# Optimization experiments

Hardware: AMD Instinct MI355X
Metric: run time of the kernel (lower is better)

## Reference

```python
import jax, jax.numpy as jnp
import numpy as np


def fps(xyz, npoint):
    # xyz: [B, N, 3] -> idx [B, npoint]; iterative farthest point sampling (start at index 0)
    B, N, _ = xyz.shape
    dist0 = jnp.full((B, N), 1e10, xyz.dtype)
    far0 = jnp.zeros((B,), jnp.int32)
    def body(carry, _):
        dist, far = carry
        centroid = jnp.take_along_axis(xyz, far[:, None, None], axis=1)  # [B,1,3]
        d = jnp.sum((xyz - centroid) ** 2, axis=-1)                      # [B,N]
        dist = jnp.minimum(dist, d)
        return (dist, jnp.argmax(dist, axis=-1).astype(jnp.int32)), far
    _, idx = jax.lax.scan(body, (dist0, far0), None, length=npoint)
    return idx.T  # [B, npoint]


def ball_query(radius, nsample, xyz, new_xyz):
    # xyz [B,N,3], new_xyz [B,S,3] -> idx [B,S,nsample]
    B, S, _ = new_xyz.shape
    N = xyz.shape[1]
    sqr = jnp.sum((new_xyz[:, :, None, :] - xyz[:, None, :, :]) ** 2, axis=-1)  # [B,S,N]
    idx = jnp.broadcast_to(jnp.arange(N, dtype=jnp.int32), (B, S, N))
    idx = jnp.where(sqr > radius * radius, N, idx)
    idx = jnp.sort(idx, axis=-1)[:, :, :nsample]
    first = idx[:, :, :1]
    return jnp.where(idx == N, first, idx)


def index_points(points, idx):
    # points [B,N,C], idx [B,...] int -> [B,...,C]
    B = points.shape[0]
    out = jnp.take_along_axis(points, idx.reshape(B, -1, 1), axis=1)
    return out.reshape(idx.shape + (points.shape[-1],))


def set_abstraction(xyz, points, npoint, radius, nsample, ws, bs):
    fidx = fps(xyz, npoint)
    new_xyz = index_points(xyz, fidx)                       # [B,S,3]
    gidx = ball_query(radius, nsample, xyz, new_xyz)        # [B,S,ns]
    grouped = index_points(xyz, gidx) - new_xyz[:, :, None, :]  # centered neighbors
    if points is not None:
        grouped = jnp.concatenate([grouped, index_points(points, gidx)], axis=-1)
    x = grouped                                             # [B,S,ns,Cin]
    for w, b in zip(ws, bs):  # shared 1x1-conv MLP (eval-mode BN folded into w,b) + ReLU
        x = jax.nn.relu(jnp.einsum('bsnc,oc->bsno', x, w) + b)
    return new_xyz, jnp.max(x, axis=2)                      # max-pool over neighbors


def sa_group_all(xyz, points, ws, bs):
    x = jnp.concatenate([xyz, points], axis=-1)             # [B,N,3+C]
    for w, b in zip(ws, bs):
        x = jax.nn.relu(jnp.einsum('bnc,oc->bno', x, w) + b)
    return jnp.max(x, axis=1)                               # [B,1024]


def setup_inputs() -> dict:
    key = jax.random.key(0)
    ks = iter(jax.random.split(key, 64))
    def w(shape):
        return jax.random.normal(next(ks), shape, jnp.float32) * 0.02
    d = {"xyz": jax.random.normal(next(ks), (32, 3, 4096), jnp.float32)}
    mlps = {"s1": [(64, 3), (64, 64), (128, 64)],
            "s2": [(128, 131), (128, 128), (256, 128)],
            "s3": [(256, 259), (512, 256), (1024, 512)]}
    for name, layers in mlps.items():
        for i, (o, c) in enumerate(layers):
            d[name + "w" + str(i)] = w((o, c))
            d[name + "b" + str(i)] = jnp.zeros((o,), jnp.float32)
    for name, (o, c) in {"f1": (512, 1024), "f2": (256, 512), "f3": (6, 256)}.items():
        d[name + "w"] = w((o, c))
        d[name + "b"] = jnp.zeros((o,), jnp.float32)
    return d


def reference(xyz, s1w0, s1b0, s1w1, s1b1, s1w2, s1b2,
              s2w0, s2b0, s2w1, s2b1, s2w2, s2b2,
              s3w0, s3b0, s3w1, s3b1, s3w2, s3b2,
              f1w, f1b, f2w, f2b, f3w, f3b):
    pts = jnp.transpose(xyz, (0, 2, 1))  # [B,N,3]
    l1x, l1p = set_abstraction(pts, None, 512, 0.2, 32, [s1w0, s1w1, s1w2], [s1b0, s1b1, s1b2])
    l2x, l2p = set_abstraction(l1x, l1p, 128, 0.4, 64, [s2w0, s2w1, s2w2], [s2b0, s2b1, s2b2])
    feat = sa_group_all(l2x, l2p, [s3w0, s3w1, s3w2], [s3b0, s3b1, s3b2])  # [B,1024]
    x = jax.nn.relu(feat @ f1w.T + f1b)   # fc1 + (folded BN) + ReLU; dropout=identity (eval)
    x = jax.nn.relu(x @ f2w.T + f2b)
    return x @ f3w.T + f3b                # [B,6] value head (softmax=False)
```

## Files before the change

kernel.cpp:

```cpp
#include <hip/hip_runtime.h>
#include <hip/hip_bf16.h>


typedef __attribute__((ext_vector_type(8))) short short8;
typedef __attribute__((ext_vector_type(4))) float f32x4;
union SV8 { short8 v; ushort u[8]; };

__device__ __forceinline__ ushort f2bf(float x) {
    unsigned u = __float_as_uint(x);
    unsigned r = (u + 0x7fffu + ((u >> 16) & 1u)) >> 16;
    return (ushort)r;
}

template<int CTRL>
__device__ __forceinline__ unsigned long long dpp_mov_u64(unsigned long long x) {
    const int lo = (int)(unsigned)(x & 0xffffffffull);
    const int hi = (int)(unsigned)(x >> 32);
    const int nlo = __builtin_amdgcn_update_dpp(lo, lo, CTRL, 0xf, 0xf, false);
    const int nhi = __builtin_amdgcn_update_dpp(hi, hi, CTRL, 0xf, 0xf, false);
    return ((unsigned long long)(unsigned)nhi << 32) | (unsigned)nlo;
}

__device__ __forceinline__ unsigned long long wave_max_u64(unsigned long long x) {
    unsigned long long y;
    y = dpp_mov_u64<0x111>(x); if (y > x) x = y;
    y = dpp_mov_u64<0x112>(x); if (y > x) x = y;
    y = dpp_mov_u64<0x114>(x); if (y > x) x = y;
    y = dpp_mov_u64<0x118>(x); if (y > x) x = y;
    y = dpp_mov_u64<0x142>(x); if (y > x) x = y;
    y = dpp_mov_u64<0x143>(x); if (y > x) x = y;
    return x;
}

template<int N, int S, int NT, bool CHW>
__device__ __forceinline__ void fps_body(const float* __restrict__ xyz,
                                         float* __restrict__ new_xyz,
                                         int b, int t, char* smem) {
    constexpr int P  = N / NT;
    constexpr int NW = NT / 64;
    float4* sxyz = (float4*)smem;
    unsigned long long* rv = (unsigned long long*)(smem + (size_t)N * 16);
    int* sfar = (int*)(smem + (size_t)N * 16 + 2 * NW * 8);
    float px[P], py[P], pz[P], dist[P];
    unsigned idc[P];
    if (CHW) {
        const float* base = xyz + (size_t)b * 3 * N;
        #pragma unroll
        for (int p = 0; p < P; ++p) {
            const int i = p * NT + t;
            px[p] = base[i]; py[p] = base[N + i]; pz[p] = base[2 * N + i];
            sxyz[i] = make_float4(px[p], py[p], pz[p], 0.0f);
        }
    } else {
        const float* base = xyz + (size_t)b * N * 3;
        #pragma unroll
        for (int p = 0; p < P; ++p) {
            const int i = p * NT + t;
            px[p] = base[i*3]; py[p] = base[i*3+1]; pz[p] = base[i*3+2];
            sxyz[i] = make_float4(px[p], py[p], pz[p], 0.0f);
        }
    }
    #pragma unroll
    for (int p = 0; p < P; ++p) { dist[p] = 1e10f; idc[p] = (unsigned)(N - 1 - (p * NT + t)); }
    __syncthreads();
    int far = 0;
    for (int j = 0; j < S; ++j) {
        if (t == 0) sfar[j] = far;
        const float4 cen = sxyz[far];
        unsigned long long pk[P];
        #pragma unroll
        for (int p = 0; p < P; ++p) {
            const float dx = px[p] - cen.x, dy = py[p] - cen.y, dz = pz[p] - cen.z;
            const float d = __fadd_rn(__fadd_rn(__fmul_rn(dx, dx), __fmul_rn(dy, dy)), __fmul_rn(dz, dz));
            const float nd = fminf(dist[p], d);
            dist[p] = nd;
            pk[p] = ((unsigned long long)__float_as_uint(nd) << 32) | idc[p];
        }
        #pragma unroll
        for (int s = P / 2; s > 0; s >>= 1)
            #pragma unroll
            for (int k = 0; k < s; ++k)
                if (pk[k + s] > pk[k]) pk[k] = pk[k + s];
        unsigned long long best = wave_max_u64(pk[0]);
        if constexpr (NW > 1) {
            const int sl = (j & 1) * NW;
            if ((t & 63) == 63) rv[sl + (t >> 6)] = best;
            __syncthreads();
            unsigned long long bb = rv[sl];
            #pragma unroll
            for (int w = 1; w < NW; ++w) { const unsigned long long v = rv[sl + w]; if (v > bb) bb = v; }
            far = N - 1 - (int)(bb & 0xffffffffull);
        } else {
            far = N - 1 - __builtin_amdgcn_readlane((int)(best & 0xffffffffull), 63);
        }
    }
    __syncthreads();
    float* out = new_xyz + (size_t)b * S * 3;
    for (int i = t; i < S; i += NT) {
        const float4 c = sxyz[sfar[i]];
        out[i*3+0] = c.x; out[i*3+1] = c.y; out[i*3+2] = c.z;
    }
}

__device__ __forceinline__ void packg(const float* __restrict__ src,
                                      ushort* __restrict__ dh,
                                      int Ktot, int otiles, int cofs, int idx) {
    const int j = idx & 7, lane = (idx >> 3) & 63;
    const int ot = (idx >> 9) % otiles;
    const int ks = idx / (512 * otiles);
    const int m = lane & 15, q = lane >> 4;
    const int o = ot * 16 + m, c = cofs + ks * 32 + q * 8 + j;
    const float v = (c < Ktot) ? src[(size_t)o * Ktot + c] : 0.0f;
    dh[idx] = f2bf(v);
}

__global__ __launch_bounds__(256)
void fps1_prep_kernel(const float* __restrict__ xyz, float* __restrict__ l1xyz,
                 const float* s1w0, const float* s1b0, float4* Wc1,
                 const float* s1w1, ushort* M1W1h,
                 const float* s1w2, ushort* M1W2h,
                 const float* s3w0, ushort* S3W0h,
                 const float* s3w1, ushort* S3W1h,
                 const float* s3w2, ushort* S3W2h,
                 const float* s2w0, const float* s2b0, float4* Wc0,
                 ushort* W0h,
                 const float* s2w1, ushort* W1h,
                 const float* s2w2, ushort* W2h) {
    __shared__ __align__(16) char smem[4096 * 16 + 64 + 512 * 4];
    if (blockIdx.x < 32) {
        fps_body<4096, 512, 256, true>(xyz, l1xyz, blockIdx.x, threadIdx.x, smem);
        return;
    }
    int i = (blockIdx.x - 32) * 256 + threadIdx.x;
    if (i < 64)     { Wc1[i] = make_float4(s1w0[i*3], s1w0[i*3+1], s1w0[i*3+2], s1b0[i]); return; }  i -= 64;
    if (i < 4096)   { packg(s1w1, M1W1h,  64,  4, 0, i); return; }   i -= 4096;
    if (i < 8192)   { packg(s1w2, M1W2h,  64,  8, 0, i); return; }   i -= 8192;
    if (i < 73728)  { packg(s3w0, S3W0h, 259, 16, 0, i); return; }   i -= 73728;
    if (i < 131072) { packg(s3w1, S3W1h, 256, 32, 0, i); return; }   i -= 131072;
    if (i < 524288) { packg(s3w2, S3W2h, 512, 64, 0, i); return; }   i -= 524288;
    if (i < 16384)  { packg(s2w0, W0h, 131,  8, 3, i); return; }     i -= 16384;
    if (i < 16384)  { packg(s2w1, W1h, 128,  8, 0, i); return; }     i -= 16384;
    if (i < 32768)  { packg(s2w2, W2h, 128, 16, 0, i); return; }     i -= 32768;
    if (i < 128) {
        Wc0[i] = make_float4(s2w0[(size_t)i*131+0], s2w0[(size_t)i*131+1],
                             s2w0[(size_t)i*131+2], s2b0[i]);
    }
}

template<int N, int NS, bool CHW, int NT>
__global__ __launch_bounds__(NT)
void bq_kernel(float r2, const float* __restrict__ xyz, const float* __restrict__ cen,
               int* __restrict__ gidx, int S) {
    constexpr int WPB = NT / 64;
    __shared__ __align__(16) float4 sp[N];
    const int t = threadIdx.x, lane = t & 63, w = t >> 6;
    const int cen0 = blockIdx.x * WPB;
    const int b = cen0 / S;
    if (CHW) {
        const float* base = xyz + (size_t)b * 3 * N;
        for (int i = t; i < N; i += NT)
            sp[i] = make_float4(base[i], base[N + i], base[2 * N + i], 0.0f);
    } else {
        const float* base = xyz + (size_t)b * N * 3;
        for (int i = t; i < N; i += NT)
            sp[i] = make_float4(base[i*3], base[i*3+1], base[i*3+2], 0.0f);
    }
    __syncthreads();
    const int wid = cen0 + w;
    const float cx = cen[(size_t)wid*3+0], cy = cen[(size_t)wid*3+1], cz = cen[(size_t)wid*3+2];
    int* out = gidx + (size_t)wid * NS;
    int cnt = 0, first = -1;
    for (int b0 = 0; b0 < N; b0 += 64) {
        const float4 p = sp[b0 + lane];
        const float dx = p.x - cx, dy = p.y - cy, dz = p.z - cz;
        const float d = __fadd_rn(__fadd_rn(__fmul_rn(dx, dx), __fmul_rn(dy, dy)), __fmul_rn(dz, dz));
        const bool in = (d <= r2);
        const unsigned long long m = __ballot(in);
        if (first < 0 && m != 0ull) first = b0 + __ffsll((unsigned long long)m) - 1;
        const int pos = cnt + (int)__popcll(m & ((1ull << lane) - 1ull));
        if (in && pos < NS) out[pos] = b0 + lane;
        cnt += (int)__popcll(m);
        if (cnt >= NS) break;
    }
    if (cnt < NS)
        for (int k = cnt + lane; k < NS; k += 64) out[k] = first;
}

__global__ __launch_bounds__(256)
void mlp1_kernel(const float* __restrict__ xyz, const float* __restrict__ l1xyz,
                 float* __restrict__ l2xyz,
                 const int* __restrict__ gidx, const float4* __restrict__ Wc1,
                 const ushort* __restrict__ W1h, const float* __restrict__ b1,
                 const ushort* __restrict__ W2h, const float* __restrict__ b2,
                 float* __restrict__ l1p) {
    __shared__ __align__(16) char smem[64 * 68 * 4 * 2];
    float* bufA = (float*)smem;
    float* bufB = (float*)(smem + 64 * 68 * 4);
    const int t = threadIdx.x, b = blockIdx.y;
    if (blockIdx.x == 256) {
        fps_body<512, 128, 256, false>(l1xyz, l2xyz, b, t, smem);
        return;
    }
    const int s0 = blockIdx.x * 2;
    {
        const int n = t >> 2, c = t & 3;
        const int s = s0 + (n >> 5);
        const int gi = gidx[((size_t)b * 512 + s) * 32 + (n & 31)];
        float v = 0.0f;
        if (c < 3) v = xyz[(size_t)b * 3 * 4096 + c * 4096 + gi] - l1xyz[((size_t)b * 512 + s) * 3 + c];
        bufB[n * 4 + c] = v;
    }
    __syncthreads();
    {
        const int o = t & 63, ng = t >> 6;
        const float4 wc = Wc1[o];
        #pragma unroll
        for (int r = 0; r < 16; ++r) {
            const int n = ng * 16 + r;
            const float z = wc.w + wc.x * bufB[n*4] + wc.y * bufB[n*4+1] + wc.z * bufB[n*4+2];
            bufA[n * 68 + o] = fmaxf(z, 0.0f);
        }
    }
    const int lane = t & 63, wv = t >> 6;
    const int m = lane & 15, q = lane >> 4;
    const int rowA = wv * 16 + m;
    f32x4 acc1[4];
    #pragma unroll
    for (int ot = 0; ot < 4; ++ot)
        #pragma unroll
        for (int r = 0; r < 4; ++r) acc1[ot][r] = 0.0f;
    #pragma unroll
    for (int ks = 0; ks < 2; ++ks) {
        float xv[8];
        *(float4*)&xv[0] = *(const float4*)&bufA[rowA * 68 + ks * 32 + q * 8];
        *(float4*)&xv[4] = *(const float4*)&bufA[rowA * 68 + ks * 32 + q * 8 + 4];
        SV8 ah;
        #pragma unroll
        for (int j = 0; j < 8; ++j) ah.u[j] = f2bf(xv[j]);
        #pragma unroll
        for (int ot = 0; ot < 4; ++ot) {
            SV8 bh;
            bh.v = *(const short8*)(W1h + (size_t)((ks * 4 + ot) * 64 + lane) * 8);
            acc1[ot] = __builtin_amdgcn_mfma_f32_16x16x32_bf16(ah.v, bh.v, acc1[ot], 0, 0, 0);
        }
    }
    #pragma unroll
    for (int ot = 0; ot < 4; ++ot) {
        const float bb = b1[ot * 16 + m];
        #pragma unroll
        for (int r = 0; r < 4; ++r)
            bufB[(wv * 16 + q * 4 + r) * 68 + ot * 16 + m] = fmaxf(acc1[ot][r] + bb, 0.0f);
    }
    f32x4 acc2[8];
    #pragma unroll
    for (int ot = 0; ot < 8; ++ot)
        #pragma unroll
        for (int r = 0; r < 4; ++r) acc2[ot][r] = 0.0f;
    #pragma unroll
    for (int ks = 0; ks < 2; ++ks) {
        float xv[8];
        *(float4*)&xv[0] = *(const float4*)&bufB[rowA * 68 + ks * 32 + q * 8];
        *(float4*)&xv[4] = *(const float4*)&bufB[rowA * 68 + ks * 32 + q * 8 + 4];
        SV8 ah;
        #pragma unroll
        for (int j = 0; j < 8; ++j) ah.u[j] = f2bf(xv[j]);
        #pragma unroll
        for (int ot = 0; ot < 8; ++ot) {
            SV8 bh;
            bh.v = *(const short8*)(W2h + (size_t)((ks * 8 + ot) * 64 + lane) * 8);
            acc2[ot] = __builtin_amdgcn_mfma_f32_16x16x32_bf16(ah.v, bh.v, acc2[ot], 0, 0, 0);
        }
    }
    __syncthreads();
    #pragma unroll
    for (int ot = 0; ot < 8; ++ot) {
        const float bb = b2[ot * 16 + m];
        float mx = 0.0f;
        #pragma unroll
        for (int r = 0; r < 4; ++r) mx = fmaxf(mx, acc2[ot][r] + bb);
        bufA[(wv * 4 + q) * 128 + ot * 16 + m] = mx;
    }
    __syncthreads();
    {
        const int half = t >> 7, o = t & 127;
        float v = bufA[(half * 8) * 128 + o];
        #pragma unroll
        for (int rr = 1; rr < 8; ++rr) v = fmaxf(v, bufA[(half * 8 + rr) * 128 + o]);
        l1p[((size_t)b * 512 + s0 + half) * 128 + o] = v;
    }
}

__global__ __launch_bounds__(256)
void mlp2_kernel(const float* __restrict__ l1xyz, const float* __restrict__ l1p,
                 const float* __restrict__ l2xyz, const int* __restrict__ gidx,
                 const ushort* __restrict__ W0h, const float4* __restrict__ Wc0,
                 const ushort* __restrict__ W1h, const float* __restrict__ b1,
                 const ushort* __restrict__ W2h, const float* __restrict__ b2,
                 float* __restrict__ X3) {
    __shared__ __align__(16) float Abuf[64 * 132];
    __shared__ __align__(16) float Bbuf[64 * 132];
    __shared__ int sg[64];
    const int t = threadIdx.x, bs = blockIdx.x, b = bs >> 7;
    if (t < 64) sg[t] = gidx[(size_t)bs * 64 + t];
    if (t < 3)  X3[(size_t)bs * 288 + t] = l2xyz[(size_t)bs * 3 + t];
    if (t >= 64 && t < 93) X3[(size_t)bs * 288 + 259 + (t - 64)] = 0.0f;
    __syncthreads();
    for (int i = t; i < 64 * 32; i += 256) {
        const int n = i >> 5, cc = i & 31;
        *(float4*)&Abuf[n * 132 + cc * 4] =
            *(const float4*)&l1p[((size_t)b * 512 + sg[n]) * 128 + cc * 4];
    }
    if (t < 192) {
        const int n = t / 3, c = t % 3;
        Abuf[n * 132 + 128 + c] =
            l1xyz[((size_t)b * 512 + sg[n]) * 3 + c] - l2xyz[(size_t)bs * 3 + c];
    }
    __syncthreads();
    const int lane = t & 63, wv = t >> 6;
    const int m = lane & 15, q = lane >> 4;
    const int rowA = wv * 16 + m;

    f32x4 acc0[8];
    #pragma unroll
    for (int ot = 0; ot < 8; ++ot)
        #pragma unroll
        for (int r = 0; r < 4; ++r) acc0[ot][r] = 0.0f;
    #pragma unroll
    for (int ks = 0; ks < 4; ++ks) {
        float xv[8];
        *(float4*)&xv[0] = *(const float4*)&Abuf[rowA * 132 + ks * 32 + q * 8];
        *(float4*)&xv[4] = *(const float4*)&Abuf[rowA * 132 + ks * 32 + q * 8 + 4];
        SV8 ah;
        #pragma unroll
        for (int j = 0; j < 8; ++j) ah.u[j] = f2bf(xv[j]);
        #pragma unroll
        for (int ot = 0; ot < 8; ++ot) {
            SV8 bh;
            bh.v = *(const short8*)(W0h + (size_t)((ks * 8 + ot) * 64 + lane) * 8);
            acc0[ot] = __builtin_amdgcn_mfma_f32_16x16x32_bf16(ah.v, bh.v, acc0[ot], 0, 0, 0);
        }
    }
    float crd[4][3];
    #pragma unroll
    for (int r = 0; r < 4; ++r) {
        const int n = wv * 16 + q * 4 + r;
        crd[r][0] = Abuf[n * 132 + 128];
        crd[r][1] = Abuf[n * 132 + 129];
        crd[r][2] = Abuf[n * 132 + 130];
    }
    #pragma unroll
    for (int ot = 0; ot < 8; ++ot) {
        const float4 wc = Wc0[ot * 16 + m];
        #pragma unroll
        for (int r = 0; r < 4; ++r) {
            const float v = acc0[ot][r] + wc.w + wc.x * crd[r][0] + wc.y * crd[r][1] + wc.z * crd[r][2];
            Bbuf[(wv * 16 + q * 4 + r) * 132 + ot * 16 + m] = fmaxf(v, 0.0f);
        }
    }
    __syncthreads();

    f32x4 acc1[8];
    #pragma unroll
    for (int ot = 0; ot < 8; ++ot)
        #pragma unroll
        for (int r = 0; r < 4; ++r) acc1[ot][r] = 0.0f;
    #pragma unroll
    for (int ks = 0; ks < 4; ++ks) {
        float xv[8];
        *(float4*)&xv[0] = *(const float4*)&Bbuf[rowA * 132 + ks * 32 + q * 8];
        *(float4*)&xv[4] = *(const float4*)&Bbuf[rowA * 132 + ks * 32 + q * 8 + 4];
        SV8 ah;
        #pragma unroll
        for (int j = 0; j < 8; ++j) ah.u[j] = f2bf(xv[j]);
        #pragma unroll
        for (int ot = 0; ot < 8; ++ot) {
            SV8 bh;
            bh.v = *(const short8*)(W1h + (size_t)((ks * 8 + ot) * 64 + lane) * 8);
            acc1[ot] = __builtin_amdgcn_mfma_f32_16x16x32_bf16(ah.v, bh.v, acc1[ot], 0, 0, 0);
        }
    }
    __syncthreads();
    #pragma unroll
    for (int ot = 0; ot < 8; ++ot) {
        const float bb = b1[ot * 16 + m];
        #pragma unroll
        for (int r = 0; r < 4; ++r)
            Abuf[(wv * 16 + q * 4 + r) * 132 + ot * 16 + m] = fmaxf(acc1[ot][r] + bb, 0.0f);
    }
    __syncthreads();

    f32x4 acc2[16];
    #pragma unroll
    for (int ot = 0; ot < 16; ++ot)
        #pragma unroll
        for (int r = 0; r < 4; ++r) acc2[ot][r] = 0.0f;
    #pragma unroll
    for (int ks = 0; ks < 4; ++ks) {
        float xv[8];
        *(float4*)&xv[0] = *(const float4*)&Abuf[rowA * 132 + ks * 32 + q * 8];
        *(float4*)&xv[4] = *(const float4*)&Abuf[rowA * 132 + ks * 32 + q * 8 + 4];
        SV8 ah;
        #pragma unroll
        for (int j = 0; j < 8; ++j) ah.u[j] = f2bf(xv[j]);
        #pragma unroll
        for (int ot = 0; ot < 16; ++ot) {
            SV8 bh;
            bh.v = *(const short8*)(W2h + (size_t)((ks * 16 + ot) * 64 + lane) * 8);
            acc2[ot] = __builtin_amdgcn_mfma_f32_16x16x32_bf16(ah.v, bh.v, acc2[ot], 0, 0, 0);
        }
    }
    __syncthreads();
    #pragma unroll
    for (int ot = 0; ot < 16; ++ot) {
        const float bb = b2[ot * 16 + m];
        float mx = 0.0f;
        #pragma unroll
        for (int r = 0; r < 4; ++r) mx = fmaxf(mx, acc2[ot][r] + bb);
        Bbuf[(wv * 4 + q) * 256 + ot * 16 + m] = mx;
    }
    __syncthreads();
    {
        float v = Bbuf[t];
        #pragma unroll
        for (int rr = 1; rr < 16; ++rr) v = fmaxf(v, Bbuf[rr * 256 + t]);
        X3[(size_t)bs * 288 + 3 + t] = v;
    }
}

template<int KSTEPS, int OTILES, bool MAXOUT>
__global__ __launch_bounds__(256)
void gemm_mfma_kernel(const float* __restrict__ A, int AS,
                      const ushort* __restrict__ Wh,
                      const float* __restrict__ bias, float* __restrict__ C, int O) {
    __shared__ float part[16][OTILES * 16];
    const int t = threadIdx.x, lane = t & 63, wv = t >> 6;
    const int m = lane & 15, q = lane >> 4;
    const int rowA = blockIdx.x * 64 + wv * 16 + m;
    const int bo = blockIdx.y, OT = O >> 4;
    f32x4 acc[OTILES];
    #pragma unroll
    for (int ot = 0; ot < OTILES; ++ot)
        #pragma unroll
        for (int r = 0; r < 4; ++r) acc[ot][r] = 0.0f;
    for (int ks = 0; ks < KSTEPS; ++ks) {
        float xv[8];
        *(float4*)&xv[0] = *(const float4*)&A[(size_t)rowA * AS + ks * 32 + q * 8];
        *(float4*)&xv[4] = *(const float4*)&A[(size_t)rowA * AS + ks * 32 + q * 8 + 4];
        SV8 ah;
        #pragma unroll
        for (int j = 0; j < 8; ++j) ah.u[j] = f2bf(xv[j]);
        #pragma unroll
        for (int ot = 0; ot < OTILES; ++ot) {
            const size_t wb = (size_t)((ks * OT + bo * OTILES + ot) * 64 + lane) * 8;
            SV8 bh;
            bh.v = *(const short8*)(Wh + wb);
            acc[ot] = __builtin_amdgcn_mfma_f32_16x16x32_bf16(ah.v, bh.v, acc[ot], 0, 0, 0);
        }
    }
    if (!MAXOUT) {
        #pragma unroll
        for (int ot = 0; ot < OTILES; ++ot) {
            const int col = (bo * OTILES + ot) * 16 + m;
            const float bb = bias[col];
            #pragma unroll
            for (int r = 0; r < 4; ++r) {
                const int row = blockIdx.x * 64 + wv * 16 + q * 4 + r;
                C[(size_t)row * O + col] = fmaxf(acc[ot][r] + bb, 0.0f);
            }
        }
    } else {
        #pragma unroll
        for (int ot = 0; ot < OTILES; ++ot) {
            const int col = (bo * OTILES + ot) * 16 + m;
            const float bb = bias[col];
            float mx = 0.0f;
            #pragma unroll
            for (int r = 0; r < 4; ++r) mx = fmaxf(mx, acc[ot][r] + bb);
            part[wv * 4 + q][ot * 16 + m] = mx;
        }
        __syncthreads();
        for (int o = t; o < OTILES * 16; o += 256) {
            float v = part[0][o];
            #pragma unroll
            for (int rr = 1; rr < 16; ++rr) v = fmaxf(v, part[rr][o]);
            C[(size_t)blockIdx.x * O + bo * OTILES * 16 + o] = v;
        }
    }
}

__global__ __launch_bounds__(256)
void fchead_kernel(const float* __restrict__ P3,
                   const float* __restrict__ f1w, const float* __restrict__ f1b,
                   const float* __restrict__ f2w, const float* __restrict__ f2b,
                   const float* __restrict__ f3w, const float* __restrict__ f3b,
                   float* __restrict__ out) {
    __shared__ __align__(16) float x[1024];
    __shared__ __align__(16) float h1[512];
    __shared__ __align__(16) float h2[256];
    const int t = threadIdx.x, b = blockIdx.x;
    for (int i = t; i < 1024; i += 256)
        x[i] = fmaxf(P3[(size_t)(2*b)*1024 + i], P3[(size_t)(2*b+1)*1024 + i]);
    __syncthreads();
    #pragma unroll
    for (int oo = 0; oo < 2; ++oo) {
        const int o = t + oo * 256;
        const float4* wr = (const float4*)(f1w + (size_t)o * 1024);
        float s0 = 0, s1 = 0, s2 = 0, s3 = 0;
        for (int c = 0; c < 256; ++c) {
            const float4 w4 = wr[c];
            const float4 xv = *(const float4*)&x[c * 4];
            s0 += w4.x * xv.x; s1 += w4.y * xv.y; s2 += w4.z * xv.z; s3 += w4.w * xv.w;
        }
        h1[o] = fmaxf(f1b[o] + ((s0 + s1) + (s2 + s3)), 0.0f);
    }
    __syncthreads();
    {
        const float4* wr = (const float4*)(f2w + (size_t)t * 512);
        float s0 = 0, s1 = 0, s2 = 0, s3 = 0;
        for (int c = 0; c < 128; ++c) {
            const float4 w4 = wr[c];
            const float4 xv = *(const float4*)&h1[c * 4];
            s0 += w4.x * xv.x; s1 += w4.y * xv.y; s2 += w4.z * xv.z; s3 += w4.w * xv.w;
        }
        h2[t] = fmaxf(f2b[t] + ((s0 + s1) + (s2 + s3)), 0.0f);
    }
    __syncthreads();
    if (t < 6) {
        const float4* wr = (const float4*)(f3w + (size_t)t * 256);
        float s0 = 0, s1 = 0, s2 = 0, s3 = 0;
        for (int c = 0; c < 64; ++c) {
            const float4 w4 = wr[c];
            const float4 xv = *(const float4*)&h2[c * 4];
            s0 += w4.x * xv.x; s1 += w4.y * xv.y; s2 += w4.z * xv.z; s3 += w4.w * xv.w;
        }
        out[b * 6 + t] = f3b[t] + ((s0 + s1) + (s2 + s3));
    }
}

extern "C" void kernel_launch(void* const* d_in, const int* in_sizes, int n_in,
                              void* d_out, int out_size, void* d_ws, size_t ws_size,
                              hipStream_t stream) {
    const float* xyz  = (const float*)d_in[0];
    const float* s1w0 = (const float*)d_in[1];  const float* s1b0 = (const float*)d_in[2];
    const float* s1w1 = (const float*)d_in[3];  const float* s1b1 = (const float*)d_in[4];
    const float* s1w2 = (const float*)d_in[5];  const float* s1b2 = (const float*)d_in[6];
    const float* s2w0 = (const float*)d_in[7];  const float* s2b0 = (const float*)d_in[8];
    const float* s2w1 = (const float*)d_in[9];  const float* s2b1 = (const float*)d_in[10];
    const float* s2w2 = (const float*)d_in[11]; const float* s2b2 = (const float*)d_in[12];
    const float* s3w0 = (const float*)d_in[13]; const float* s3b0 = (const float*)d_in[14];
    const float* s3w1 = (const float*)d_in[15]; const float* s3b1 = (const float*)d_in[16];
    const float* s3w2 = (const float*)d_in[17]; const float* s3b2 = (const float*)d_in[18];
    const float* f1w  = (const float*)d_in[19]; const float* f1b  = (const float*)d_in[20];
    const float* f2w  = (const float*)d_in[21]; const float* f2b  = (const float*)d_in[22];
    const float* f3w  = (const float*)d_in[23]; const float* f3b  = (const float*)d_in[24];

    char* ws = (char*)d_ws;
    float* l1_xyz = (float*)(ws + 0);
    int*   gidx1  = (int*)  (ws + 196608);
    float* l1p    = (float*)(ws + 2293760);
    float* l2_xyz = (float*)(ws + 10682368);
    int*   gidx2  = (int*)  (ws + 10731520);
    float* X3p    = (float*)(ws + 11780096);
    const size_t PK = 16498688;
    float4* Wc1   = (float4*)(ws + PK + 0);
    ushort* M1W1h = (ushort*)(ws + PK + 1024);
    ushort* M1W2h = (ushort*)(ws + PK + 17408);
    ushort* W0h   = (ushort*)(ws + PK + 50176);
    ushort* W1h   = (ushort*)(ws + PK + 115712);
    ushort* W2h   = (ushort*)(ws + PK + 181248);
    float4* Wc0   = (float4*)(ws + PK + 312320);
    ushort* S3W0h = (ushort*)(ws + PK + 314368);
    ushort* S3W1h = (ushort*)(ws + PK + 609280);
    ushort* S3W2h = (ushort*)(ws + PK + 1133568);
    float* Y1   = (float*)(ws + 19729408);
    float* Y2   = (float*)(ws + 23923712);
    float* P3   = (float*)(ws + 32312320);

    fps1_prep_kernel<<<3186, 256, 0, stream>>>(xyz, l1_xyz,
        s1w0, s1b0, Wc1, s1w1, M1W1h, s1w2, M1W2h,
        s3w0, S3W0h, s3w1, S3W1h, s3w2, S3W2h,
        s2w0, s2b0, Wc0, W0h, s2w1, W1h, s2w2, W2h);
    bq_kernel<4096, 32, true, 1024><<<1024, 1024, 0, stream>>>(
        (float)(0.2 * 0.2), xyz, l1_xyz, gidx1, 512);
    {
        dim3 g(257, 32);
        mlp1_kernel<<<g, 256, 0, stream>>>(xyz, l1_xyz, l2_xyz, gidx1,
            Wc1, M1W1h, s1b1, M1W2h, s1b2, l1p);
    }

    bq_kernel<512, 64, false, 1024><<<256, 1024, 0, stream>>>(
        (float)(0.4 * 0.4), l1_xyz, l2_xyz, gidx2, 128);
    mlp2_kernel<<<4096, 256, 0, stream>>>(l1_xyz, l1p, l2_xyz, gidx2,
        W0h, Wc0, W1h, s2b1, W2h, s2b2, X3p);

    {
        dim3 g1(64, 4);
        gemm_mfma_kernel<9,  4, false><<<g1, 256, 0, stream>>>(X3p, 288, S3W0h, s3b0, Y1, 256);
        dim3 g2(64, 8);
        gemm_mfma_kernel<8,  4, false><<<g2, 256, 0, stream>>>(Y1, 256, S3W1h, s3b1, Y2, 512);
        dim3 g3(64, 16);
        gemm_mfma_kernel<16, 4, true ><<<g3, 256, 0, stream>>>(Y2, 512, S3W2h, s3b2, P3, 1024);
    }

    fchead_kernel<<<32, 256, 0, stream>>>(P3, f1w, f1b, f2w, f2b, f3w, f3b, (float*)d_out);
    (void)in_sizes; (void)n_in; (void)out_size; (void)ws_size;
}
```

Baseline: 783.0 us.

## Fuse three group-all MLP GEMMs into one kernel with LDS-resident bf16 intermediates

Replaces three separate MFMA GEMM launches for the global set-abstraction MLP with a single kernel. Each block processes 64 rows through all three layers and keeps the hidden activations in shared memory as bf16. The final max-pool is written directly. This removes the global round trips for the Y1/Y2 intermediates and two launches, but shrinks the grid to 64 blocks so each block does all output channels serially with lower parallelism.

```diff
diff --git a/kernel.cpp b/kernel.cpp
--- a/kernel.cpp
+++ b/kernel.cpp
@@ -427,64 +427,116 @@
     }
 }
 
-template<int KSTEPS, int OTILES, bool MAXOUT>
 __global__ __launch_bounds__(256)
-void gemm_mfma_kernel(const float* __restrict__ A, int AS,
-                      const ushort* __restrict__ Wh,
-                      const float* __restrict__ bias, float* __restrict__ C, int O) {
-    __shared__ float part[16][OTILES * 16];
+void fused3_kernel(const float* __restrict__ A,
+                   const ushort* __restrict__ W0h, const float* __restrict__ b0,
+                   const ushort* __restrict__ W1h, const float* __restrict__ b1,
+                   const ushort* __restrict__ W2h, const float* __restrict__ b2,
+                   float* __restrict__ P3) {
+    __shared__ __align__(16) char arena[64*264*2 + 64*520*2 + 16*256*4];
+    ushort* h1 = (ushort*)arena;
+    ushort* h2 = (ushort*)(arena + 64*264*2);
+    float* part = (float*)(arena + 64*264*2 + 64*520*2);
     const int t = threadIdx.x, lane = t & 63, wv = t >> 6;
     const int m = lane & 15, q = lane >> 4;
-    const int rowA = blockIdx.x * 64 + wv * 16 + m;
-    const int bo = blockIdx.y, OT = O >> 4;
-    f32x4 acc[OTILES];
-    #pragma unroll
-    for (int ot = 0; ot < OTILES; ++ot)
-        #pragma unroll
-        for (int r = 0; r < 4; ++r) acc[ot][r] = 0.0f;
-    for (int ks = 0; ks < KSTEPS; ++ks) {
-        float xv[8];
-        *(float4*)&xv[0] = *(const float4*)&A[(size_t)rowA * AS + ks * 32 + q * 8];
-        *(float4*)&xv[4] = *(const float4*)&A[(size_t)rowA * AS + ks * 32 + q * 8 + 4];
-        SV8 ah;
-        #pragma unroll
-        for (int j = 0; j < 8; ++j) ah.u[j] = f2bf(xv[j]);
-        #pragma unroll
-        for (int ot = 0; ot < OTILES; ++ot) {
-            const size_t wb = (size_t)((ks * OT + bo * OTILES + ot) * 64 + lane) * 8;
-            SV8 bh;
-            bh.v = *(const short8*)(Wh + wb);
-            acc[ot] = __builtin_amdgcn_mfma_f32_16x16x32_bf16(ah.v, bh.v, acc[ot], 0, 0, 0);
-        }
-    }
-    if (!MAXOUT) {
-        #pragma unroll
-        for (int ot = 0; ot < OTILES; ++ot) {
-            const int col = (bo * OTILES + ot) * 16 + m;
-            const float bb = bias[col];
-            #pragma unroll
-            for (int r = 0; r < 4; ++r) {
-                const int row = blockIdx.x * 64 + wv * 16 + q * 4 + r;
-                C[(size_t)row * O + col] = fmaxf(acc[ot][r] + bb, 0.0f);
+    const int rloc = wv * 16;
+    const size_t rowA = (size_t)blockIdx.x * 64 + rloc + m;
+
+    {
+        f32x4 acc[16];
+        #pragma unroll
+        for (int ot = 0; ot < 16; ++ot)
+            #pragma unroll
+            for (int r = 0; r < 4; ++r) acc[ot][r] = 0.0f;
+        #pragma unroll
+        for (int ks = 0; ks < 9; ++ks) {
+            float xv[8];
+            *(float4*)&xv[0] = *(const float4*)&A[rowA * 288 + ks * 32 + q * 8];
+            *(float4*)&xv[4] = *(const float4*)&A[rowA * 288 + ks * 32 + q * 8 + 4];
+            SV8 ah;
+            #pragma unroll
+            for (int j = 0; j < 8; ++j) ah.u[j] = f2bf(xv[j]);
+            #pragma unroll
+            for (int ot = 0; ot < 16; ++ot) {
+                SV8 bh;
+                bh.v = *(const short8*)(W0h + (size_t)((ks * 16 + ot) * 64 + lane) * 8);
+                acc[ot] = __builtin_amdgcn_mfma_f32_16x16x32_bf16(ah.v, bh.v, acc[ot], 0, 0, 0);
             }
         }
-    } else {
-        #pragma unroll
-        for (int ot = 0; ot < OTILES; ++ot) {
-            const int col = (bo * OTILES + ot) * 16 + m;
-            const float bb = bias[col];
+        #pragma unroll
+        for (int ot = 0; ot < 16; ++ot) {
+            const float bb = b0[ot * 16 + m];
+            #pragma unroll
+            for (int r = 0; r < 4; ++r)
+                h1[(rloc + q * 4 + r) * 264 + ot * 16 + m] = f2bf(fmaxf(acc[ot][r] + bb, 0.0f));
+        }
+    }
+    __syncthreads();
+
+    #pragma unroll
+    for (int og = 0; og < 2; ++og) {
+        f32x4 acc[16];
+        #pragma unroll
+        for (int ot = 0; ot < 16; ++ot)
+            #pragma unroll
+            for (int r = 0; r < 4; ++r) acc[ot][r] = 0.0f;
+        #pragma unroll
+        for (int ks = 0; ks < 8; ++ks) {
+            SV8 ah;
+            ah.v = *(const short8*)(h1 + (rloc + m) * 264 + ks * 32 + q * 8);
+            #pragma unroll
+            for (int ot = 0; ot < 16; ++ot) {
+                const int cot = og * 16 + ot;
+                SV8 bh;
+                bh.v = *(const short8*)(W1h + (size_t)((ks * 32 + cot) * 64 + lane) * 8);
+                acc[ot] = __builtin_amdgcn_mfma_f32_16x16x32_bf16(ah.v, bh.v, acc[ot], 0, 0, 0);
+            }
+        }
+        #pragma unroll
+        for (int ot = 0; ot < 16; ++ot) {
+            const int co = (og * 16 + ot) * 16 + m;
+            const float bb = b1[co];
+            #pragma unroll
+            for (int r = 0; r < 4; ++r)
+                h2[(rloc + q * 4 + r) * 520 + co] = f2bf(fmaxf(acc[ot][r] + bb, 0.0f));
+        }
+    }
+    __syncthreads();
+
+    for (int og = 0; og < 4; ++og) {
+        f32x4 acc[16];
+        #pragma unroll
+        for (int ot = 0; ot < 16; ++ot)
+            #pragma unroll
+            for (int r = 0; r < 4; ++r) acc[ot][r] = 0.0f;
+        #pragma unroll
+        for (int ks = 0; ks < 16; ++ks) {
+            SV8 ah;
+            ah.v = *(const short8*)(h2 + (rloc + m) * 520 + ks * 32 + q * 8);
+            #pragma unroll
+            for (int ot = 0; ot < 16; ++ot) {
+                const int cot = og * 16 + ot;
+                SV8 bh;
+                bh.v = *(const short8*)(W2h + (size_t)((ks * 64 + cot) * 64 + lane) * 8);
+                acc[ot] = __builtin_amdgcn_mfma_f32_16x16x32_bf16(ah.v, bh.v, acc[ot], 0, 0, 0);
+            }
+        }
+        #pragma unroll
+        for (int ot = 0; ot < 16; ++ot) {
+            const float bb = b2[(og * 16 + ot) * 16 + m];
             float mx = 0.0f;
             #pragma unroll
             for (int r = 0; r < 4; ++r) mx = fmaxf(mx, acc[ot][r] + bb);
-            part[wv * 4 + q][ot * 16 + m] = mx;
+            part[(wv * 4 + q) * 256 + ot * 16 + m] = mx;
         }
         __syncthreads();
-        for (int o = t; o < OTILES * 16; o += 256) {
-            float v = part[0][o];
-            #pragma unroll
-            for (int rr = 1; rr < 16; ++rr) v = fmaxf(v, part[rr][o]);
-            C[(size_t)blockIdx.x * O + bo * OTILES * 16 + o] = v;
-        }
+        {
+            float v = part[t];
+            #pragma unroll
+            for (int rr = 1; rr < 16; ++rr) v = fmaxf(v, part[rr * 256 + t]);
+            P3[(size_t)blockIdx.x * 1024 + og * 256 + t] = v;
+        }
+        __syncthreads();
     }
 }
 
@@ -572,8 +624,6 @@
     ushort* S3W0h = (ushort*)(ws + PK + 314368);
     ushort* S3W1h = (ushort*)(ws + PK + 609280);
     ushort* S3W2h = (ushort*)(ws + PK + 1133568);
-    float* Y1   = (float*)(ws + 19729408);
-    float* Y2   = (float*)(ws + 23923712);
     float* P3   = (float*)(ws + 32312320);
 
     fps1_prep_kernel<<<3186, 256, 0, stream>>>(xyz, l1_xyz,
@@ -593,14 +643,8 @@
     mlp2_kernel<<<4096, 256, 0, stream>>>(l1_xyz, l1p, l2_xyz, gidx2,
         W0h, Wc0, W1h, s2b1, W2h, s2b2, X3p);
 
-    {
-        dim3 g1(64, 4);
-        gemm_mfma_kernel<9,  4, false><<<g1, 256, 0, stream>>>(X3p, 288, S3W0h, s3b0, Y1, 256);
-        dim3 g2(64, 8);
-        gemm_mfma_kernel<8,  4, false><<<g2, 256, 0, stream>>>(Y1, 256, S3W1h, s3b1, Y2, 512);
-        dim3 g3(64, 16);
-        gemm_mfma_kernel<16, 4, true ><<<g3, 256, 0, stream>>>(Y2, 512, S3W2h, s3b2, P3, 1024);
-    }
+    fused3_kernel<<<64, 256, 0, stream>>>(X3p, S3W0h, s3b0, S3W1h, s3b1,
+                                          S3W2h, s3b2, P3);
 
     fchead_kernel<<<32, 256, 0, stream>>>(P3, f1w, f1b, f2w, f2b, f3w, f3b, (float*)d_out);
     (void)in_sizes; (void)n_in; (void)out_size; (void)ws_size;
```

Result: slower. 833.2 us (+6.4%).

## Fuse level-2 ball query into mlp2 and merge tail GEMMs into a cooperative kernel

Applied to the files above, without the earlier changes.

The level-2 ball query is now done inside mlp2_kernel. Each block stages the batch's 512 level-1 points in shared memory and builds its 64 neighbor indices with a wave ballot/prefix scan, so the separate bq_kernel launch and the gidx2 round-trip through global memory go away. The three SA3 GEMMs and the FC head are merged into one cooperative kernel of 256 blocks, with grid.sync between stages, replacing four launches. The trade-off is that each mlp2 block repeats the point scan, the tail has less parallelism per stage, and it depends on cooperative launch and grid-wide barriers.

```diff
diff --git a/kernel.cpp b/kernel.cpp
--- a/kernel.cpp
+++ b/kernel.cpp
@@ -1,5 +1,8 @@
 #include <hip/hip_runtime.h>
 #include <hip/hip_bf16.h>
+#include <hip/hip_cooperative_groups.h>
+
+namespace cg = cooperative_groups;
 
 
 typedef __attribute__((ext_vector_type(8))) short short8;
@@ -292,7 +295,7 @@
 
 __global__ __launch_bounds__(256)
 void mlp2_kernel(const float* __restrict__ l1xyz, const float* __restrict__ l1p,
-                 const float* __restrict__ l2xyz, const int* __restrict__ gidx,
+                 const float* __restrict__ l2xyz,
                  const ushort* __restrict__ W0h, const float4* __restrict__ Wc0,
                  const ushort* __restrict__ W1h, const float* __restrict__ b1,
                  const ushort* __restrict__ W2h, const float* __restrict__ b2,
@@ -300,10 +303,35 @@
     __shared__ __align__(16) float Abuf[64 * 132];
     __shared__ __align__(16) float Bbuf[64 * 132];
     __shared__ int sg[64];
+    __shared__ __align__(16) float4 sp4[512];
     const int t = threadIdx.x, bs = blockIdx.x, b = bs >> 7;
-    if (t < 64) sg[t] = gidx[(size_t)bs * 64 + t];
+    {
+        const float* base = l1xyz + (size_t)b * 512 * 3;
+        for (int i = t; i < 512; i += 256)
+            sp4[i] = make_float4(base[i*3], base[i*3+1], base[i*3+2], 0.0f);
+    }
     if (t < 3)  X3[(size_t)bs * 288 + t] = l2xyz[(size_t)bs * 3 + t];
     if (t >= 64 && t < 93) X3[(size_t)bs * 288 + 259 + (t - 64)] = 0.0f;
+    __syncthreads();
+    if (t < 64) {
+        const float r2 = (float)(0.4 * 0.4);
+        const float cx = l2xyz[(size_t)bs*3+0], cy = l2xyz[(size_t)bs*3+1], cz = l2xyz[(size_t)bs*3+2];
+        int cnt = 0, first = -1;
+        for (int b0 = 0; b0 < 512; b0 += 64) {
+            const float4 p = sp4[b0 + t];
+            const float dx = p.x - cx, dy = p.y - cy, dz = p.z - cz;
+            const float d = __fadd_rn(__fadd_rn(__fmul_rn(dx, dx), __fmul_rn(dy, dy)), __fmul_rn(dz, dz));
+            const bool in = (d <= r2);
+            const unsigned long long mm = __ballot(in);
+            if (first < 0 && mm != 0ull) first = b0 + __ffsll((unsigned long long)mm) - 1;
+            const int pos = cnt + (int)__popcll(mm & ((1ull << t) - 1ull));
+            if (in && pos < 64) sg[pos] = b0 + t;
+            cnt += (int)__popcll(mm);
+            if (cnt >= 64) break;
+        }
+        if (cnt < 64)
+            for (int k = cnt + t; k < 64; k += 64) sg[k] = first;
+    }
     __syncthreads();
     for (int i = t; i < 64 * 32; i += 256) {
         const int n = i >> 5, cc = i & 31;
@@ -312,8 +340,9 @@
     }
     if (t < 192) {
         const int n = t / 3, c = t % 3;
-        Abuf[n * 132 + 128 + c] =
-            l1xyz[((size_t)b * 512 + sg[n]) * 3 + c] - l2xyz[(size_t)bs * 3 + c];
+        const float4 pp = sp4[sg[n]];
+        const float pc = (c == 0) ? pp.x : (c == 1) ? pp.y : pp.z;
+        Abuf[n * 132 + 128 + c] = pc - l2xyz[(size_t)bs * 3 + c];
     }
     __syncthreads();
     const int lane = t & 63, wv = t >> 6;
@@ -427,19 +456,17 @@
     }
 }
 
-template<int KSTEPS, int OTILES, bool MAXOUT>
-__global__ __launch_bounds__(256)
-void gemm_mfma_kernel(const float* __restrict__ A, int AS,
-                      const ushort* __restrict__ Wh,
-                      const float* __restrict__ bias, float* __restrict__ C, int O) {
-    __shared__ float part[16][OTILES * 16];
-    const int t = threadIdx.x, lane = t & 63, wv = t >> 6;
-    const int m = lane & 15, q = lane >> 4;
-    const int rowA = blockIdx.x * 64 + wv * 16 + m;
-    const int bo = blockIdx.y, OT = O >> 4;
-    f32x4 acc[OTILES];
-    #pragma unroll
-    for (int ot = 0; ot < OTILES; ++ot)
+__device__ __forceinline__ void gemm_tile4(const float* __restrict__ A, int AS,
+                                           const ushort* __restrict__ Wh,
+                                           const float* __restrict__ bias,
+                                           float* __restrict__ C, int O,
+                                           int KSTEPS, int rt, int bo,
+                                           int lane, int wv, int m, int q) {
+    const int rowA = rt * 64 + wv * 16 + m;
+    const int OT = O >> 4;
+    f32x4 acc[4];
+    #pragma unroll
+    for (int ot = 0; ot < 4; ++ot)
         #pragma unroll
         for (int r = 0; r < 4; ++r) acc[ot][r] = 0.0f;
     for (int ks = 0; ks < KSTEPS; ++ks) {
@@ -450,56 +477,100 @@
         #pragma unroll
         for (int j = 0; j < 8; ++j) ah.u[j] = f2bf(xv[j]);
         #pragma unroll
-        for (int ot = 0; ot < OTILES; ++ot) {
-            const size_t wb = (size_t)((ks * OT + bo * OTILES + ot) * 64 + lane) * 8;
+        for (int ot = 0; ot < 4; ++ot) {
+            const size_t wb = (size_t)((ks * OT + bo * 4 + ot) * 64 + lane) * 8;
             SV8 bh;
             bh.v = *(const short8*)(Wh + wb);
             acc[ot] = __builtin_amdgcn_mfma_f32_16x16x32_bf16(ah.v, bh.v, acc[ot], 0, 0, 0);
         }
     }
-    if (!MAXOUT) {
-        #pragma unroll
-        for (int ot = 0; ot < OTILES; ++ot) {
-            const int col = (bo * OTILES + ot) * 16 + m;
-            const float bb = bias[col];
+    #pragma unroll
+    for (int ot = 0; ot < 4; ++ot) {
+        const int col = (bo * 4 + ot) * 16 + m;
+        const float bb = bias[col];
+        #pragma unroll
+        for (int r = 0; r < 4; ++r) {
+            const int row = rt * 64 + wv * 16 + q * 4 + r;
+            C[(size_t)row * O + col] = fmaxf(acc[ot][r] + bb, 0.0f);
+        }
+    }
+}
+
+__global__ __launch_bounds__(256)
+void tail_coop_kernel(const float* __restrict__ X3,
+                      const ushort* __restrict__ W0h, const float* __restrict__ b0,
+                      const ushort* __restrict__ W1h, const float* __restrict__ b1,
+                      const ushort* __restrict__ W2h, const float* __restrict__ b2,
+                      float* __restrict__ Y1, float* __restrict__ Y2,
+                      float* __restrict__ P3,
+                      const float* __restrict__ f1w, const float* __restrict__ f1b,
+                      const float* __restrict__ f2w, const float* __restrict__ f2b,
+                      const float* __restrict__ f3w, const float* __restrict__ f3b,
+                      float* __restrict__ out) {
+    cg::grid_group grid = cg::this_grid();
+    __shared__ float part[16][64];
+    __shared__ __align__(16) float xb[1024];
+    __shared__ __align__(16) float h1b[512];
+    __shared__ __align__(16) float h2b[256];
+    const int t = threadIdx.x, lane = t & 63, wv = t >> 6;
+    const int m = lane & 15, q = lane >> 4;
+    const int bid = blockIdx.x;
+    const int rt = bid >> 2, bq4 = bid & 3;
+
+    gemm_tile4(X3, 288, W0h, b0, Y1, 256, 9, rt, bq4, lane, wv, m, q);
+    grid.sync();
+
+    #pragma unroll
+    for (int j = 0; j < 2; ++j)
+        gemm_tile4(Y1, 256, W1h, b1, Y2, 512, 8, rt, bq4 * 2 + j, lane, wv, m, q);
+    grid.sync();
+
+    for (int j = 0; j < 4; ++j) {
+        const int bo = bq4 * 4 + j;
+        f32x4 acc[4];
+        #pragma unroll
+        for (int ot = 0; ot < 4; ++ot)
             #pragma unroll
-            for (int r = 0; r < 4; ++r) {
-                const int row = blockIdx.x * 64 + wv * 16 + q * 4 + r;
-                C[(size_t)row * O + col] = fmaxf(acc[ot][r] + bb, 0.0f);
+            for (int r = 0; r < 4; ++r) acc[ot][r] = 0.0f;
+        const int rowA = rt * 64 + wv * 16 + m;
+        for (int ks = 0; ks < 16; ++ks) {
+            float xv[8];
+            *(float4*)&xv[0] = *(const float4*)&Y2[(size_t)rowA * 512 + ks * 32 + q * 8];
+            *(float4*)&xv[4] = *(const float4*)&Y2[(size_t)rowA * 512 + ks * 32 + q * 8 + 4];
+            SV8 ah;
+            #pragma unroll
+            for (int jj = 0; jj < 8; ++jj) ah.u[jj] = f2bf(xv[jj]);
+            #pragma unroll
+            for (int ot = 0; ot < 4; ++ot) {
+                const size_t wb = (size_t)((ks * 64 + bo * 4 + ot) * 64 + lane) * 8;
+                SV8 bh;
+                bh.v = *(const short8*)(W2h + wb);
+                acc[ot] = __builtin_amdgcn_mfma_f32_16x16x32_bf16(ah.v, bh.v, acc[ot], 0, 0, 0);
             }
         }
-    } else {
-        #pragma unroll
-        for (int ot = 0; ot < OTILES; ++ot) {
-            const int col = (bo * OTILES + ot) * 16 + m;
-            const float bb = bias[col];
+        #pragma unroll
+        for (int ot = 0; ot < 4; ++ot) {
+            const float bb = b2[(bo * 4 + ot) * 16 + m];
             float mx = 0.0f;
             #pragma unroll
             for (int r = 0; r < 4; ++r) mx = fmaxf(mx, acc[ot][r] + bb);
             part[wv * 4 + q][ot * 16 + m] = mx;
         }
         __syncthreads();
-        for (int o = t; o < OTILES * 16; o += 256) {
+        for (int o = t; o < 64; o += 256) {
             float v = part[0][o];
             #pragma unroll
             for (int rr = 1; rr < 16; ++rr) v = fmaxf(v, part[rr][o]);
-            C[(size_t)blockIdx.x * O + bo * OTILES * 16 + o] = v;
-        }
-    }
-}
-
-__global__ __launch_bounds__(256)
-void fchead_kernel(const float* __restrict__ P3,
-                   const float* __restrict__ f1w, const float* __restrict__ f1b,
-                   const float* __restrict__ f2w, const float* __restrict__ f2b,
-                   const float* __restrict__ f3w, const float* __restrict__ f3b,
-                   float* __restrict__ out) {
-    __shared__ __align__(16) float x[1024];
-    __shared__ __align__(16) float h1[512];
-    __shared__ __align__(16) float h2[256];
-    const int t = threadIdx.x, b = blockIdx.x;
+            P3[(size_t)rt * 1024 + bo * 64 + o] = v;
+        }
+        __syncthreads();
+    }
+    grid.sync();
+
+    if (bid >= 32) return;
+    const int b = bid;
     for (int i = t; i < 1024; i += 256)
-        x[i] = fmaxf(P3[(size_t)(2*b)*1024 + i], P3[(size_t)(2*b+1)*1024 + i]);
+        xb[i] = fmaxf(P3[(size_t)(2*b)*1024 + i], P3[(size_t)(2*b+1)*1024 + i]);
     __syncthreads();
     #pragma unroll
     for (int oo = 0; oo < 2; ++oo) {
@@ -508,10 +579,10 @@
         float s0 = 0, s1 = 0, s2 = 0, s3 = 0;
         for (int c = 0; c < 256; ++c) {
             const float4 w4 = wr[c];
-            const float4 xv = *(const float4*)&x[c * 4];
+            const float4 xv = *(const float4*)&xb[c * 4];
             s0 += w4.x * xv.x; s1 += w4.y * xv.y; s2 += w4.z * xv.z; s3 += w4.w * xv.w;
         }
-        h1[o] = fmaxf(f1b[o] + ((s0 + s1) + (s2 + s3)), 0.0f);
+        h1b[o] = fmaxf(f1b[o] + ((s0 + s1) + (s2 + s3)), 0.0f);
     }
     __syncthreads();
     {
@@ -519,10 +590,10 @@
         float s0 = 0, s1 = 0, s2 = 0, s3 = 0;
         for (int c = 0; c < 128; ++c) {
             const float4 w4 = wr[c];
-            const float4 xv = *(const float4*)&h1[c * 4];
+            const float4 xv = *(const float4*)&h1b[c * 4];
             s0 += w4.x * xv.x; s1 += w4.y * xv.y; s2 += w4.z * xv.z; s3 += w4.w * xv.w;
         }
-        h2[t] = fmaxf(f2b[t] + ((s0 + s1) + (s2 + s3)), 0.0f);
+        h2b[t] = fmaxf(f2b[t] + ((s0 + s1) + (s2 + s3)), 0.0f);
     }
     __syncthreads();
     if (t < 6) {
@@ -530,7 +601,7 @@
         float s0 = 0, s1 = 0, s2 = 0, s3 = 0;
         for (int c = 0; c < 64; ++c) {
             const float4 w4 = wr[c];
-            const float4 xv = *(const float4*)&h2[c * 4];
+            const float4 xv = *(const float4*)&h2b[c * 4];
             s0 += w4.x * xv.x; s1 += w4.y * xv.y; s2 += w4.z * xv.z; s3 += w4.w * xv.w;
         }
         out[b * 6 + t] = f3b[t] + ((s0 + s1) + (s2 + s3));
@@ -559,7 +630,6 @@
     int*   gidx1  = (int*)  (ws + 196608);
     float* l1p    = (float*)(ws + 2293760);
     float* l2_xyz = (float*)(ws + 10682368);
-    int*   gidx2  = (int*)  (ws + 10731520);
     float* X3p    = (float*)(ws + 11780096);
     const size_t PK = 16498688;
     float4* Wc1   = (float4*)(ws + PK + 0);
@@ -588,20 +658,20 @@
             Wc1, M1W1h, s1b1, M1W2h, s1b2, l1p);
     }
 
-    bq_kernel<512, 64, false, 1024><<<256, 1024, 0, stream>>>(
-        (float)(0.4 * 0.4), l1_xyz, l2_xyz, gidx2, 128);
-    mlp2_kernel<<<4096, 256, 0, stream>>>(l1_xyz, l1p, l2_xyz, gidx2,
+    mlp2_kernel<<<4096, 256, 0, stream>>>(l1_xyz, l1p, l2_xyz,
         W0h, Wc0, W1h, s2b1, W2h, s2b2, X3p);
 
     {
-        dim3 g1(64, 4);
-        gemm_mfma_kernel<9,  4, false><<<g1, 256, 0, stream>>>(X3p, 288, S3W0h, s3b0, Y1, 256);
-        dim3 g2(64, 8);
-        gemm_mfma_kernel<8,  4, false><<<g2, 256, 0, stream>>>(Y1, 256, S3W1h, s3b1, Y2, 512);
-        dim3 g3(64, 16);
-        gemm_mfma_kernel<16, 4, true ><<<g3, 256, 0, stream>>>(Y2, 512, S3W2h, s3b2, P3, 1024);
-    }
-
-    fchead_kernel<<<32, 256, 0, stream>>>(P3, f1w, f1b, f2w, f2b, f3w, f3b, (float*)d_out);
+        float* dout = (float*)d_out;
+        void* args[] = {
+            (void*)&X3p, (void*)&S3W0h, (void*)&s3b0,
+            (void*)&S3W1h, (void*)&s3b1, (void*)&S3W2h, (void*)&s3b2,
+            (void*)&Y1, (void*)&Y2, (void*)&P3,
+            (void*)&f1w, (void*)&f1b, (void*)&f2w, (void*)&f2b,
+            (void*)&f3w, (void*)&f3b, (void*)&dout
+        };
+        hipLaunchCooperativeKernel((const void*)tail_coop_kernel,
+                                   dim3(256), dim3(256), args, 0, stream);
+    }
     (void)in_sizes; (void)n_in; (void)out_size; (void)ws_size;
 }
```

Result: slower. 902.3 us (+15.2%).
